# Kernel tuning notes

Hardware: AMD Instinct MI355X
Metric: run time of the kernel (lower is better)

The kernel has to match this reference:

```python
import jax, jax.numpy as jnp
import numpy as np

B, S, T, D = 64, 256, 8, 256
E, M = 500000, 2048
NEG_INF = -10000000000.0


def setup_inputs() -> dict:
    key = jax.random.key(0)
    ks = jax.random.split(key, 9)
    token_reprs = jax.random.normal(ks[0], (B, S, T, D), dtype=jnp.float32)
    w1 = jax.random.normal(ks[1], (D, D // 2), dtype=jnp.float32) * (1.0 / np.sqrt(D))
    b1 = jnp.zeros((D // 2,), dtype=jnp.float32)
    w2 = jax.random.normal(ks[2], (D // 2, 1), dtype=jnp.float32) * (1.0 / np.sqrt(D // 2))
    b2 = jnp.zeros((1,), dtype=jnp.float32)
    edge_index = jax.random.randint(ks[3], (2, E), 0, B * S, dtype=jnp.int32)
    lm_indices = jax.random.randint(ks[4], (M,), 0, B * S * T, dtype=jnp.int32)
    batch_pointers = jax.random.randint(ks[5], (M,), 0, B, dtype=jnp.int32)
    tree_padding_mask = jax.random.randint(ks[6], (B, S), 0, 2, dtype=jnp.int32).astype(jnp.bool_)
    return {
        "token_reprs": token_reprs,
        "w1": w1, "b1": b1, "w2": w2, "b2": b2,
        "edge_index": edge_index,
        "lm_indices": lm_indices,
        "batch_pointers": batch_pointers,
        "tree_padding_mask": tree_padding_mask,
    }


def reference(token_reprs, w1, b1, w2, b2, edge_index, lm_indices, batch_pointers, tree_padding_mask):
    b, s, t, d = token_reprs.shape
    # type representation is the first token of each type tree
    type_reprs = token_reprs[:, :, 0]                  # [B, S, D]
    flat_types = type_reprs.reshape(b * s, d)          # [B*S, D]

    # predict_lemmas: gather scope/goal reprs, elementwise multiply, 2-layer MLP
    scope_ids, goal_ids = edge_index[0], edge_index[1]
    h = flat_types[scope_ids] * flat_types[goal_ids]   # [E, D]
    h = h @ w1 + b1                                    # [E, D//2] (Dropout is identity in eval)
    lemmas = (h @ w2 + b2)[:, 0]                       # [E]

    # predict_masks: gather masked token reprs + per-tree candidates, dot, mask
    mask_reprs = token_reprs.reshape(b * s * t, d)[lm_indices]  # [M, D]
    candidates = type_reprs[batch_pointers]            # [M, S, D]
    candidate_mask = tree_padding_mask[batch_pointers] # [M, S]
    lm_preds = jnp.einsum('md,msd->ms', mask_reprs, candidates)
    lm_preds = jnp.where(candidate_mask, lm_preds, NEG_INF)
    return lemmas, lm_preds
```

## Files before the change

kernel.cpp:

```cpp
#include <hip/hip_runtime.h>

#define DD 256
#define SS 256
#define BB 64
#define NEDGE 500000
#define MM 2048
#define NEG_INF -10000000000.0f
#define ROWF4 512
#define NROWS (BB * SS)

#define OFF_VC     0
#define OFF_MSORT  4096
#define OFF_BSTART (4096 + MM * 4)
#define OFF_FSLAB  (1 << 16)
#define OFF_P2     ((1 << 16) + (4 << 20))
#define OFF_MROWS  ((1 << 16) + (12 << 20))

typedef float vf4 __attribute__((ext_vector_type(4)));
typedef float f32x2 __attribute__((ext_vector_type(2)));
typedef float f32x4 __attribute__((ext_vector_type(4)));
typedef short bf16x8 __attribute__((ext_vector_type(8)));

__device__ __forceinline__ float bflo(unsigned u) { return __uint_as_float(u << 16); }
__device__ __forceinline__ float bfhi(unsigned u) { return __uint_as_float(u & 0xFFFF0000u); }
__device__ __forceinline__ unsigned short bf_rne(float f) {
    unsigned u = __float_as_uint(f);
    return (unsigned short)((u + 0x7FFFu + ((u >> 16) & 1u)) >> 16);
}
__device__ __forceinline__ unsigned pack2_rne(float a, float b) {
    return (unsigned)bf_rne(a) | ((unsigned)bf_rne(b) << 16);
}

#if __has_builtin(__builtin_amdgcn_cvt_pk_fp8_f32) && __has_builtin(__builtin_amdgcn_cvt_pk_f32_fp8)
#define FP8_HW 1
#else
#define FP8_HW 0
#endif

__device__ __forceinline__ unsigned char sw_f32_to_e4m3(float f) {
    unsigned u = __float_as_uint(f);
    unsigned s = (u >> 24) & 0x80u;
    float af = fabsf(f);
    if (af >= 448.f) return (unsigned char)(s | 0x7E);
    if (af < 0.015625f) {
        int q = (int)(af * 512.f + 0.5f);
        return (unsigned char)(s | (unsigned)q);
    }
    unsigned lsb = (u >> 20) & 1u;
    u += 0x7FFFFu + lsb;
    int e = (int)(u >> 23) - 120;
    unsigned m = (u >> 20) & 7u;
    if (e >= 16) return (unsigned char)(s | 0x7E);
    return (unsigned char)(s | ((unsigned)e << 3) | m);
}
__device__ __forceinline__ float sw_e4m3_to_f32(unsigned b) {
    unsigned s = (b & 0x80u) << 24;
    unsigned e = (b >> 3) & 0xFu, m = b & 7u;
    if (e == 0) {
        float v = (float)m * 0.001953125f;
        return (b & 0x80u) ? -v : v;
    }
    return __uint_as_float(s | ((e + 120u) << 23) | (m << 20));
}

__device__ __forceinline__ unsigned enc_fp8x4(float x, float y, float z, float w) {
#if FP8_HW
    int r = 0;
    r = __builtin_amdgcn_cvt_pk_fp8_f32(x, y, r, false);
    r = __builtin_amdgcn_cvt_pk_fp8_f32(z, w, r, true);
    return (unsigned)r;
#else
    return (unsigned)sw_f32_to_e4m3(x) | ((unsigned)sw_f32_to_e4m3(y) << 8)
         | ((unsigned)sw_f32_to_e4m3(z) << 16) | ((unsigned)sw_f32_to_e4m3(w) << 24);
#endif
}

__device__ __forceinline__ float dot4_fp8(unsigned aw, unsigned bw, const float4 v) {
#if FP8_HW
    f32x2 al = __builtin_amdgcn_cvt_pk_f32_fp8((int)aw, false);
    f32x2 ah = __builtin_amdgcn_cvt_pk_f32_fp8((int)aw, true);
    f32x2 bl = __builtin_amdgcn_cvt_pk_f32_fp8((int)bw, false);
    f32x2 bh = __builtin_amdgcn_cvt_pk_f32_fp8((int)bw, true);
    return (al.x * bl.x) * v.x + (al.y * bl.y) * v.y
         + (ah.x * bh.x) * v.z + (ah.y * bh.y) * v.w;
#else
    return sw_e4m3_to_f32(aw & 255u) * sw_e4m3_to_f32(bw & 255u) * v.x
         + sw_e4m3_to_f32((aw >> 8) & 255u) * sw_e4m3_to_f32((bw >> 8) & 255u) * v.y
         + sw_e4m3_to_f32((aw >> 16) & 255u) * sw_e4m3_to_f32((bw >> 16) & 255u) * v.z
         + sw_e4m3_to_f32(aw >> 24) * sw_e4m3_to_f32(bw >> 24) * v.w;
#endif
}

__global__ __launch_bounds__(256) void prep(
        const float* __restrict__ tok, const int* __restrict__ lmi,
        const float* __restrict__ w1, const float* __restrict__ b1,
        const float* __restrict__ w2, const float* __restrict__ b2,
        const int* __restrict__ bp,
        unsigned* __restrict__ fslab,
        unsigned* __restrict__ p2, unsigned* __restrict__ mrows,
        float* __restrict__ vc, int* __restrict__ msorted,
        int* __restrict__ bstart) {
    const int t = threadIdx.x;
    const int lane = t & 63;
    const int w    = t >> 6;
    if (blockIdx.x < NROWS / 4) {
        const int row = blockIdx.x * 4 + w;
        const float4 a = ((const float4*)tok)[(size_t)row * ROWF4 + lane];
        fslab[(size_t)row * 64 + lane] = enc_fp8x4(a.x, a.y, a.z, a.w);
        const size_t pi = (size_t)row * 128 + lane * 2;
        p2[pi]     = pack2_rne(a.x, a.y);
        p2[pi + 1] = pack2_rne(a.z, a.w);
    } else if (blockIdx.x < NROWS / 4 + MM / 4) {
        const int m = (blockIdx.x - NROWS / 4) * 4 + w;
        const float4 a = ((const float4*)(tok + (size_t)lmi[m] * DD))[lane];
        mrows[(size_t)m * 128 + lane * 2]     = pack2_rne(a.x, a.y);
        mrows[(size_t)m * 128 + lane * 2 + 1] = pack2_rne(a.z, a.w);
    } else if (blockIdx.x == NROWS / 4 + MM / 4) {
        __shared__ float sw2[DD / 2];
        if (t < DD / 2) sw2[t] = w2[t];
        __syncthreads();
        for (int r = w; r < DD; r += 4) {
            float x = w1[r * (DD / 2) + lane] * sw2[lane]
                    + w1[r * (DD / 2) + 64 + lane] * sw2[64 + lane];
            x += __shfl_down(x, 32);
            x += __shfl_down(x, 16);
            x += __shfl_down(x, 8);
            x += __shfl_down(x, 4);
            x += __shfl_down(x, 2);
            x += __shfl_down(x, 1);
            if (lane == 0) vc[r] = x;
        }
        if (w == 0) {
            float x = b1[lane] * sw2[lane] + b1[64 + lane] * sw2[64 + lane];
            x += __shfl_down(x, 32);
            x += __shfl_down(x, 16);
            x += __shfl_down(x, 8);
            x += __shfl_down(x, 4);
            x += __shfl_down(x, 2);
            x += __shfl_down(x, 1);
            if (lane == 0) vc[DD] = x + b2[0];
        }
    } else {
        __shared__ int hist[BB];
        __shared__ int offs[BB + 1];
        if (t < BB) hist[t] = 0;
        __syncthreads();
        for (int m = t; m < MM; m += 256) atomicAdd(&hist[bp[m]], 1);
        __syncthreads();
        if (t == 0) {
            int acc = 0;
            for (int i = 0; i < BB; ++i) { offs[i] = acc; acc += hist[i]; }
            offs[BB] = acc;
        }
        __syncthreads();
        if (t < BB + 1) bstart[t] = offs[t];
        __syncthreads();
        for (int m = t; m < MM; m += 256) {
            int pos = atomicAdd(&offs[bp[m]], 1);
            msorted[pos] = m;
        }
    }
}

__global__ __launch_bounds__(256) void edge_fp8(
        const unsigned* __restrict__ fslab,
        const int* __restrict__ edges, const float* __restrict__ vc,
        float* __restrict__ out) {
    const int t = threadIdx.x;
    const int lane = t & 63, w = t >> 6;
    const int l16 = lane & 15;
    const int g = lane >> 4;
    const int e0 = blockIdx.x * 256;

    __shared__ int sIdx[2][256];
    __shared__ float accs[256];
    const int e = e0 + t;
    const bool val = e < NEDGE;
    sIdx[0][t] = val ? __builtin_nontemporal_load(edges + e) : 0;
    sIdx[1][t] = val ? __builtin_nontemporal_load(edges + NEDGE + e) : 0;

    const float4 v0 = ((const float4*)vc)[l16 * 4 + 0];
    const float4 v1 = ((const float4*)vc)[l16 * 4 + 1];
    const float4 v2 = ((const float4*)vc)[l16 * 4 + 2];
    const float4 v3 = ((const float4*)vc)[l16 * 4 + 3];
    __syncthreads();

    #pragma unroll 4
    for (int it = 0; it < 16; ++it) {
        const int slot = w * 64 + it * 4 + g;
        const int sc = sIdx[0][slot];
        const int gl = sIdx[1][slot];
        const uint4 A = *(const uint4*)(fslab + (size_t)sc * 64 + l16 * 4);
        const uint4 B = *(const uint4*)(fslab + (size_t)gl * 64 + l16 * 4);
        float s = dot4_fp8(A.x, B.x, v0) + dot4_fp8(A.y, B.y, v1)
                + dot4_fp8(A.z, B.z, v2) + dot4_fp8(A.w, B.w, v3);
        s += __shfl_down(s, 8, 16);
        s += __shfl_down(s, 4, 16);
        s += __shfl_down(s, 2, 16);
        s += __shfl_down(s, 1, 16);
        if (l16 == 0) accs[slot] = s;
    }
    __syncthreads();
    const float c = vc[DD];
    if (val) __builtin_nontemporal_store(accs[t] + c, out + e);
}

__global__ __launch_bounds__(256) void lm_gemm(
        const unsigned* __restrict__ p2,
        const unsigned* __restrict__ mrows,
        const int* __restrict__ msorted,
        const int* __restrict__ bstart,
        const int* __restrict__ tpm,
        float* __restrict__ out) {
    const int b  = blockIdx.x;
    const int st = blockIdx.y;
    const int ch = blockIdx.z;
    const int s0 = bstart[b], s1 = bstart[b + 1];
    const int base = s0 + ch * 32;
    if (base >= s1) return;
    const int nm = min(32, s1 - base);
    const int t = threadIdx.x;

    __shared__ __align__(16) unsigned lmaskU[32 * 132];
    __shared__ __align__(16) unsigned srowU[32 * 132];
    __shared__ int mids[32];
    __shared__ int sact[64];
    __shared__ int snact;

    if (t < 32) mids[t] = msorted[base + min(t, nm - 1)];
    if (t >= 64 && t < 128) {
        int lt = t - 64;
        bool act = tpm[b * SS + st * 64 + lt] != 0;
        unsigned long long mk = __ballot(act);
        if (act) sact[__popcll(mk & ((1ull << lt) - 1))] = lt;
        if (lt == 0) snact = (int)__popcll(mk);
    }
    __syncthreads();

    for (int f = t; f < nm * 32; f += 256) {
        int r = f >> 5, q = f & 31;
        *(uint4*)&lmaskU[r * 132 + q * 4] = ((const uint4*)mrows)[(size_t)mids[r] * 32 + q];
    }
    for (int f = t; f < nm * 64; f += 256) {
        int i = f >> 6, c = f & 63;
        if (!tpm[b * SS + st * 64 + c])
            out[(size_t)mids[i] * SS + st * 64 + c] = NEG_INF;
    }
    __syncthreads();

    const int nact = snact;
    const int lane = t & 63;
    const int wv = t >> 6;
    const int rt = wv >> 1;
    const int ct = wv & 1;
    const int fr = lane & 15;
    const int fq = lane >> 4;

    for (int g = 0; g * 32 < nact; ++g) {
        if (g) __syncthreads();
        const int nv = min(32, nact - g * 32);
        for (int f = t; f < nv * 32; f += 256) {
            int r = f >> 5, q = f & 31;
            size_t row = (size_t)b * SS + st * 64 + sact[g * 32 + r];
            *(uint4*)&srowU[r * 132 + q * 4] = ((const uint4*)p2)[row * 32 + q];
        }
        __syncthreads();

        f32x4 acc = {0.f, 0.f, 0.f, 0.f};
        #pragma unroll
        for (int stp = 0; stp < 8; ++stp) {
            bf16x8 a = *(const bf16x8*)&lmaskU[(rt * 16 + fr) * 132 + stp * 16 + fq * 4];
            bf16x8 bfr = *(const bf16x8*)&srowU[(ct * 16 + fr) * 132 + stp * 16 + fq * 4];
            acc = __builtin_amdgcn_mfma_f32_16x16x32_bf16(a, bfr, acc, 0, 0, 0);
        }

        const int jg = g * 32 + ct * 16 + fr;
        if (jg < nact) {
            const int sj = sact[jg];
            #pragma unroll
            for (int r = 0; r < 4; ++r) {
                const int mi = rt * 16 + fq * 4 + r;
                if (mi < nm) out[(size_t)mids[mi] * SS + st * 64 + sj] = acc[r];
            }
        }
    }
}

extern "C" void kernel_launch(void* const* d_in, const int* in_sizes, int n_in,
                              void* d_out, int out_size, void* d_ws, size_t ws_size,
                              hipStream_t stream) {
    const float* tok = (const float*)d_in[0];
    const float* w1  = (const float*)d_in[1];
    const float* b1  = (const float*)d_in[2];
    const float* w2  = (const float*)d_in[3];
    const float* b2  = (const float*)d_in[4];
    const int* edges = (const int*)d_in[5];
    const int* lmi   = (const int*)d_in[6];
    const int* bp    = (const int*)d_in[7];
    const int* tpm   = (const int*)d_in[8];

    float* out_lemmas = (float*)d_out;
    float* out_lm     = (float*)d_out + NEDGE;

    char* ws = (char*)d_ws;
    float* vc        = (float*)(ws + OFF_VC);
    int* msorted     = (int*)(ws + OFF_MSORT);
    int* bstart      = (int*)(ws + OFF_BSTART);
    unsigned* fslab  = (unsigned*)(ws + OFF_FSLAB);
    unsigned* p2     = (unsigned*)(ws + OFF_P2);
    unsigned* mrows  = (unsigned*)(ws + OFF_MROWS);

    prep<<<NROWS / 4 + MM / 4 + 2, 256, 0, stream>>>(
        tok, lmi, w1, b1, w2, b2, bp, fslab, p2, mrows, vc, msorted, bstart);
    edge_fp8<<<(NEDGE + 255) / 256, 256, 0, stream>>>(fslab, edges, vc, out_lemmas);
    lm_gemm<<<dim3(BB, 4, 8), 256, 0, stream>>>(p2, mrows, msorted, bstart, tpm, out_lm);
}
```

Baseline: 247.4 us.

## Fuse edge scoring and LM GEMM into one interleaved-block kernel

```diff
diff --git a/kernel.cpp b/kernel.cpp
--- a/kernel.cpp
+++ b/kernel.cpp
@@ -8,6 +8,10 @@
 #define NEG_INF -10000000000.0f
 #define ROWF4 512
 #define NROWS (BB * SS)
+
+#define EBLK ((NEDGE + 255) / 256)
+#define LMBLK (BB * 4 * 8)
+#define FUSE_GRID 4096
 
 #define OFF_VC     0
 #define OFF_MSORT  4096
@@ -162,125 +166,116 @@
     }
 }
 
-__global__ __launch_bounds__(256) void edge_fp8(
+__global__ __launch_bounds__(256, 8) void edge_lm(
         const unsigned* __restrict__ fslab,
         const int* __restrict__ edges, const float* __restrict__ vc,
-        float* __restrict__ out) {
-    const int t = threadIdx.x;
-    const int lane = t & 63, w = t >> 6;
-    const int l16 = lane & 15;
-    const int g = lane >> 4;
-    const int e0 = blockIdx.x * 256;
-
-    __shared__ int sIdx[2][256];
-    __shared__ float accs[256];
-    const int e = e0 + t;
-    const bool val = e < NEDGE;
-    sIdx[0][t] = val ? __builtin_nontemporal_load(edges + e) : 0;
-    sIdx[1][t] = val ? __builtin_nontemporal_load(edges + NEDGE + e) : 0;
-
-    const float4 v0 = ((const float4*)vc)[l16 * 4 + 0];
-    const float4 v1 = ((const float4*)vc)[l16 * 4 + 1];
-    const float4 v2 = ((const float4*)vc)[l16 * 4 + 2];
-    const float4 v3 = ((const float4*)vc)[l16 * 4 + 3];
-    __syncthreads();
-
-    #pragma unroll 4
-    for (int it = 0; it < 16; ++it) {
-        const int slot = w * 64 + it * 4 + g;
-        const int sc = sIdx[0][slot];
-        const int gl = sIdx[1][slot];
-        const uint4 A = *(const uint4*)(fslab + (size_t)sc * 64 + l16 * 4);
-        const uint4 B = *(const uint4*)(fslab + (size_t)gl * 64 + l16 * 4);
-        float s = dot4_fp8(A.x, B.x, v0) + dot4_fp8(A.y, B.y, v1)
-                + dot4_fp8(A.z, B.z, v2) + dot4_fp8(A.w, B.w, v3);
-        s += __shfl_down(s, 8, 16);
-        s += __shfl_down(s, 4, 16);
-        s += __shfl_down(s, 2, 16);
-        s += __shfl_down(s, 1, 16);
-        if (l16 == 0) accs[slot] = s;
-    }
-    __syncthreads();
-    const float c = vc[DD];
-    if (val) __builtin_nontemporal_store(accs[t] + c, out + e);
-}
-
-__global__ __launch_bounds__(256) void lm_gemm(
+        float* __restrict__ out_lemmas,
         const unsigned* __restrict__ p2,
         const unsigned* __restrict__ mrows,
         const int* __restrict__ msorted,
         const int* __restrict__ bstart,
         const int* __restrict__ tpm,
-        float* __restrict__ out) {
-    const int b  = blockIdx.x;
-    const int st = blockIdx.y;
-    const int ch = blockIdx.z;
-    const int s0 = bstart[b], s1 = bstart[b + 1];
-    const int base = s0 + ch * 32;
-    if (base >= s1) return;
-    const int nm = min(32, s1 - base);
+        float* __restrict__ out_lm) {
     const int t = threadIdx.x;
-
-    __shared__ __align__(16) unsigned lmaskU[32 * 132];
-    __shared__ __align__(16) unsigned srowU[32 * 132];
+    const int lane = t & 63;
+
+    __shared__ int sIdx[2][256];
+    __shared__ float accs[256];
     __shared__ int mids[32];
     __shared__ int sact[64];
     __shared__ int snact;
 
-    if (t < 32) mids[t] = msorted[base + min(t, nm - 1)];
-    if (t >= 64 && t < 128) {
-        int lt = t - 64;
-        bool act = tpm[b * SS + st * 64 + lt] != 0;
-        unsigned long long mk = __ballot(act);
-        if (act) sact[__popcll(mk & ((1ull << lt) - 1))] = lt;
-        if (lt == 0) snact = (int)__popcll(mk);
-    }
-    __syncthreads();
-
-    for (int f = t; f < nm * 32; f += 256) {
-        int r = f >> 5, q = f & 31;
-        *(uint4*)&lmaskU[r * 132 + q * 4] = ((const uint4*)mrows)[(size_t)mids[r] * 32 + q];
-    }
-    for (int f = t; f < nm * 64; f += 256) {
-        int i = f >> 6, c = f & 63;
-        if (!tpm[b * SS + st * 64 + c])
-            out[(size_t)mids[i] * SS + st * 64 + c] = NEG_INF;
-    }
-    __syncthreads();
-
-    const int nact = snact;
-    const int lane = t & 63;
-    const int wv = t >> 6;
-    const int rt = wv >> 1;
-    const int ct = wv & 1;
-    const int fr = lane & 15;
-    const int fq = lane >> 4;
-
-    for (int g = 0; g * 32 < nact; ++g) {
-        if (g) __syncthreads();
-        const int nv = min(32, nact - g * 32);
-        for (int f = t; f < nv * 32; f += 256) {
-            int r = f >> 5, q = f & 31;
-            size_t row = (size_t)b * SS + st * 64 + sact[g * 32 + r];
-            *(uint4*)&srowU[r * 132 + q * 4] = ((const uint4*)p2)[row * 32 + q];
-        }
-        __syncthreads();
-
-        f32x4 acc = {0.f, 0.f, 0.f, 0.f};
-        #pragma unroll
-        for (int stp = 0; stp < 8; ++stp) {
-            bf16x8 a = *(const bf16x8*)&lmaskU[(rt * 16 + fr) * 132 + stp * 16 + fq * 4];
-            bf16x8 bfr = *(const bf16x8*)&srowU[(ct * 16 + fr) * 132 + stp * 16 + fq * 4];
-            acc = __builtin_amdgcn_mfma_f32_16x16x32_bf16(a, bfr, acc, 0, 0, 0);
-        }
-
-        const int jg = g * 32 + ct * 16 + fr;
-        if (jg < nact) {
-            const int sj = sact[jg];
+    if ((blockIdx.x & 1) == 0) {
+        const int eb = blockIdx.x >> 1;
+        if (eb >= EBLK) return;
+        const int w = t >> 6;
+        const int l16 = lane & 15;
+        const int g = lane >> 4;
+        const int e0 = eb * 256;
+
+        const int e = e0 + t;
+        const bool val = e < NEDGE;
+        sIdx[0][t] = val ? __builtin_nontemporal_load(edges + e) : 0;
+        sIdx[1][t] = val ? __builtin_nontemporal_load(edges + NEDGE + e) : 0;
+
+        const float4 v0 = ((const float4*)vc)[l16 * 4 + 0];
+        const float4 v1 = ((const float4*)vc)[l16 * 4 + 1];
+        const float4 v2 = ((const float4*)vc)[l16 * 4 + 2];
+        const float4 v3 = ((const float4*)vc)[l16 * 4 + 3];
+        __syncthreads();
+
+        #pragma unroll 4
+        for (int it = 0; it < 16; ++it) {
+            const int slot = w * 64 + it * 4 + g;
+            const int sc = sIdx[0][slot];
+            const int gl = sIdx[1][slot];
+            const uint4 A = *(const uint4*)(fslab + (size_t)sc * 64 + l16 * 4);
+            const uint4 B = *(const uint4*)(fslab + (size_t)gl * 64 + l16 * 4);
+            float s = dot4_fp8(A.x, B.x, v0) + dot4_fp8(A.y, B.y, v1)
+                    + dot4_fp8(A.z, B.z, v2) + dot4_fp8(A.w, B.w, v3);
+            s += __shfl_down(s, 8, 16);
+            s += __shfl_down(s, 4, 16);
+            s += __shfl_down(s, 2, 16);
+            s += __shfl_down(s, 1, 16);
+            if (l16 == 0) accs[slot] = s;
+        }
+        __syncthreads();
+        const float c = vc[DD];
+        if (val) __builtin_nontemporal_store(accs[t] + c, out_lemmas + e);
+    } else {
+        const int li = blockIdx.x >> 1;
+        const int ch = li & 7;
+        const int st = (li >> 3) & 3;
+        const int b  = li >> 5;
+        const int s0 = bstart[b], s1 = bstart[b + 1];
+        const int base = s0 + ch * 32;
+        if (base >= s1) return;
+        const int nm = min(32, s1 - base);
+
+        if (t < 32) mids[t] = msorted[base + min(t, nm - 1)];
+        if (t >= 64 && t < 128) {
+            int lt = t - 64;
+            bool act = tpm[b * SS + st * 64 + lt] != 0;
+            unsigned long long mk = __ballot(act);
+            if (act) sact[__popcll(mk & ((1ull << lt) - 1))] = lt;
+            if (lt == 0) snact = (int)__popcll(mk);
+        }
+        __syncthreads();
+
+        for (int f = t; f < nm * 64; f += 256) {
+            int i = f >> 6, c = f & 63;
+            if (!tpm[b * SS + st * 64 + c])
+                out_lm[(size_t)mids[i] * SS + st * 64 + c] = NEG_INF;
+        }
+
+        const int nact = snact;
+        const int wv = t >> 6;
+        const int rt = wv >> 1;
+        const int ct = wv & 1;
+        const int fr = lane & 15;
+        const int fq = lane >> 4;
+
+        const size_t arow = (size_t)mids[rt * 16 + fr] * 128;
+
+        for (int g = 0; g * 32 < nact; ++g) {
+            const int jg = g * 32 + ct * 16 + fr;
+            const int sj = sact[min(jg, nact - 1)];
+            const size_t brow = ((size_t)b * SS + st * 64 + sj) * 128;
+
+            f32x4 acc = {0.f, 0.f, 0.f, 0.f};
             #pragma unroll
-            for (int r = 0; r < 4; ++r) {
-                const int mi = rt * 16 + fq * 4 + r;
-                if (mi < nm) out[(size_t)mids[mi] * SS + st * 64 + sj] = acc[r];
+            for (int stp = 0; stp < 8; ++stp) {
+                bf16x8 a  = *(const bf16x8*)&mrows[arow + stp * 16 + fq * 4];
+                bf16x8 bf = *(const bf16x8*)&p2[brow + stp * 16 + fq * 4];
+                acc = __builtin_amdgcn_mfma_f32_16x16x32_bf16(a, bf, acc, 0, 0, 0);
+            }
+
+            if (jg < nact) {
+                #pragma unroll
+                for (int r = 0; r < 4; ++r) {
+                    const int mi = rt * 16 + fq * 4 + r;
+                    if (mi < nm) out_lm[(size_t)mids[mi] * SS + st * 64 + sj] = acc[r];
+                }
             }
         }
     }
@@ -312,6 +307,6 @@
 
     prep<<<NROWS / 4 + MM / 4 + 2, 256, 0, stream>>>(
         tok, lmi, w1, b1, w2, b2, bp, fslab, p2, mrows, vc, msorted, bstart);
-    edge_fp8<<<(NEDGE + 255) / 256, 256, 0, stream>>>(fslab, edges, vc, out_lemmas);
-    lm_gemm<<<dim3(BB, 4, 8), 256, 0, stream>>>(p2, mrows, msorted, bstart, tpm, out_lm);
-}
+    edge_lm<<<FUSE_GRID, 256, 0, stream>>>(
+        fslab, edges, vc, out_lemmas, p2, mrows, msorted, bstart, tpm, out_lm);
+}
```

Measured after the change: 260.7 us. 1.05x slower.
